# Optimization experiments

Hardware: AMD Instinct MI355X
Metric: run time of the kernel (lower is better)

Reference implementation:

```python
import jax, jax.numpy as jnp
import numpy as np

B = 4096          # batch_size (pairs); 2B total rows
D = 512           # embedding dim
TEMPERATURE = 0.5 # registered buffer in the torch module
EPS = 1e-12       # F.normalize eps


def _l2_normalize(x):
    # torch F.normalize: x / max(||x||_2, eps)
    n = jnp.sqrt(jnp.sum(x * x, axis=1, keepdims=True))
    return x / jnp.maximum(n, EPS)


def setup_inputs() -> dict:
    key = jax.random.key(0)
    k1, k2 = jax.random.split(key)
    return {
        "emb_i": jax.random.normal(k1, (B, D), dtype=jnp.float32),
        "emb_j": jax.random.normal(k2, (B, D), dtype=jnp.float32),
    }


def reference(emb_i, emb_j):
    z_i = _l2_normalize(emb_i)                     # [B, D]
    z_j = _l2_normalize(emb_j)                     # [B, D]
    z = jnp.concatenate([z_i, z_j], axis=0)        # [2B, D]
    # cosine similarity of normalized rows == plain GEMM (instead of the
    # broadcasted unsqueeze in the original, same math)
    sim = z @ z.T                                  # [2B, 2B]
    positives = jnp.concatenate(
        [jnp.diagonal(sim, offset=B), jnp.diagonal(sim, offset=-B)], axis=0
    )                                              # [2B]
    nominator = jnp.exp(positives / TEMPERATURE)   # [2B]
    # NOTE: the original multiplies exp(sim/T) by an *identity* mask (a bug
    # w.r.t. SimCLR, but we reproduce it faithfully): the row-sum of
    # eye * exp(sim/T) is exactly exp(diag(sim)/T).
    denominator = jnp.exp(jnp.diagonal(sim) / TEMPERATURE)  # [2B]
    loss_partial = -jnp.log(nominator / denominator)         # [2B]
    loss = jnp.sum(loss_partial) / (2 * B)
    return loss
```

## Files before the change

### kernel.cpp

```cpp
#include <hip/hip_runtime.h>
#include <hip/hip_bf16.h>


#define BATCH 4096
#define DIM 512
#define ROWS_PER_BLOCK 4
#define NBLOCKS (BATCH / ROWS_PER_BLOCK)

__global__ void pair_cosine_partial(const float* __restrict__ a,
                                    const float* __restrict__ b,
                                    float* __restrict__ partial) {
    const int wave = threadIdx.x >> 6;
    const int lane = threadIdx.x & 63;
    const int row  = blockIdx.x * ROWS_PER_BLOCK + wave;

    const float4* a4 = reinterpret_cast<const float4*>(a) + (size_t)row * (DIM / 4);
    const float4* b4 = reinterpret_cast<const float4*>(b) + (size_t)row * (DIM / 4);

    float4 av0 = a4[lane];
    float4 av1 = a4[lane + 64];
    float4 bv0 = b4[lane];
    float4 bv1 = b4[lane + 64];

    float dot = av0.x * bv0.x + av0.y * bv0.y + av0.z * bv0.z + av0.w * bv0.w
              + av1.x * bv1.x + av1.y * bv1.y + av1.z * bv1.z + av1.w * bv1.w;
    float na  = av0.x * av0.x + av0.y * av0.y + av0.z * av0.z + av0.w * av0.w
              + av1.x * av1.x + av1.y * av1.y + av1.z * av1.z + av1.w * av1.w;
    float nb  = bv0.x * bv0.x + bv0.y * bv0.y + bv0.z * bv0.z + bv0.w * bv0.w
              + bv1.x * bv1.x + bv1.y * bv1.y + bv1.z * bv1.z + bv1.w * bv1.w;

    #pragma unroll
    for (int off = 32; off > 0; off >>= 1) {
        dot += __shfl_xor(dot, off);
        na  += __shfl_xor(na, off);
        nb  += __shfl_xor(nb, off);
    }

    __shared__ float s[ROWS_PER_BLOCK];
    if (lane == 0) {
        float denom = fmaxf(sqrtf(na), 1e-12f) * fmaxf(sqrtf(nb), 1e-12f);
        s[wave] = dot / denom;
    }
    __syncthreads();
    if (threadIdx.x == 0) {
        partial[blockIdx.x] = s[0] + s[1] + s[2] + s[3];
    }
}

__global__ void finalize_loss(const float* __restrict__ partial,
                              float* __restrict__ out) {
    const int t = threadIdx.x;
    float v = partial[t] + partial[t + 256] + partial[t + 512] + partial[t + 768];
    #pragma unroll
    for (int off = 32; off > 0; off >>= 1) {
        v += __shfl_xor(v, off);
    }
    __shared__ float s[4];
    if ((t & 63) == 0) s[t >> 6] = v;
    __syncthreads();
    if (t == 0) {
        float sum_p = s[0] + s[1] + s[2] + s[3];
        float mean_p = sum_p / (float)BATCH;
        out[0] = (1.0f - mean_p) * 2.0f;
    }
}

extern "C" void kernel_launch(void* const* d_in, const int* in_sizes, int n_in,
                              void* d_out, int out_size, void* d_ws, size_t ws_size,
                              hipStream_t stream) {
    const float* a = (const float*)d_in[0];
    const float* b = (const float*)d_in[1];
    float* out = (float*)d_out;
    float* partial = (float*)d_ws;

    pair_cosine_partial<<<NBLOCKS, 256, 0, stream>>>(a, b, partial);
    finalize_loss<<<1, 256, 0, stream>>>(partial, out);
}
```

Baseline: 11.41 us.

## Fuse partial and finalize kernels via cooperative grid sync

Merges the per-pair cosine kernel and the final reduction kernel into one cooperative kernel that uses a grid-wide sync before block 0 reduces the partials. Blocks grow to 1024 threads, 16 rows each, so 256 blocks are launched. The aim is to remove the second launch and its gap. In exchange it pays for a grid barrier and the cost of a cooperative launch, and it needs all 256 blocks to be co-resident on the GPU.

```diff
diff --git a/kernel.cpp b/kernel.cpp
--- a/kernel.cpp
+++ b/kernel.cpp
@@ -1,18 +1,23 @@
 #include <hip/hip_runtime.h>
-#include <hip/hip_bf16.h>
+#include <hip/hip_cooperative_groups.h>
+
+namespace cg = cooperative_groups;
 
 
 #define BATCH 4096
 #define DIM 512
-#define ROWS_PER_BLOCK 4
-#define NBLOCKS (BATCH / ROWS_PER_BLOCK)
+#define THREADS 1024
+#define WAVES_PER_BLOCK 16
+#define NBLOCKS (BATCH / WAVES_PER_BLOCK)
 
-__global__ void pair_cosine_partial(const float* __restrict__ a,
-                                    const float* __restrict__ b,
-                                    float* __restrict__ partial) {
+__global__ void __launch_bounds__(THREADS)
+fused_contrastive_loss(const float* __restrict__ a,
+                       const float* __restrict__ b,
+                       float* __restrict__ out,
+                       float* __restrict__ partial) {
     const int wave = threadIdx.x >> 6;
     const int lane = threadIdx.x & 63;
-    const int row  = blockIdx.x * ROWS_PER_BLOCK + wave;
+    const int row  = blockIdx.x * WAVES_PER_BLOCK + wave;
 
     const float4* a4 = reinterpret_cast<const float4*>(a) + (size_t)row * (DIM / 4);
     const float4* b4 = reinterpret_cast<const float4*>(b) + (size_t)row * (DIM / 4);
@@ -36,32 +41,37 @@
         nb  += __shfl_xor(nb, off);
     }
 
-    __shared__ float s[ROWS_PER_BLOCK];
+    __shared__ float s[WAVES_PER_BLOCK];
     if (lane == 0) {
         float denom = fmaxf(sqrtf(na), 1e-12f) * fmaxf(sqrtf(nb), 1e-12f);
         s[wave] = dot / denom;
     }
     __syncthreads();
     if (threadIdx.x == 0) {
-        partial[blockIdx.x] = s[0] + s[1] + s[2] + s[3];
+        float p = 0.f;
+        #pragma unroll
+        for (int i = 0; i < WAVES_PER_BLOCK; ++i) p += s[i];
+        partial[blockIdx.x] = p;
     }
-}
 
-__global__ void finalize_loss(const float* __restrict__ partial,
-                              float* __restrict__ out) {
-    const int t = threadIdx.x;
-    float v = partial[t] + partial[t + 256] + partial[t + 512] + partial[t + 768];
-    #pragma unroll
-    for (int off = 32; off > 0; off >>= 1) {
-        v += __shfl_xor(v, off);
-    }
-    __shared__ float s[4];
-    if ((t & 63) == 0) s[t >> 6] = v;
-    __syncthreads();
-    if (t == 0) {
-        float sum_p = s[0] + s[1] + s[2] + s[3];
-        float mean_p = sum_p / (float)BATCH;
-        out[0] = (1.0f - mean_p) * 2.0f;
+    cg::this_grid().sync();
+
+    if (blockIdx.x == 0) {
+        float v = (threadIdx.x < NBLOCKS) ? partial[threadIdx.x] : 0.0f;
+        #pragma unroll
+        for (int off = 32; off > 0; off >>= 1) {
+            v += __shfl_xor(v, off);
+        }
+        __shared__ float s2[WAVES_PER_BLOCK];
+        if (lane == 0) s2[wave] = v;
+        __syncthreads();
+        if (threadIdx.x == 0) {
+            float sum_p = 0.f;
+            #pragma unroll
+            for (int i = 0; i < WAVES_PER_BLOCK; ++i) sum_p += s2[i];
+            float mean_p = sum_p / (float)BATCH;
+            out[0] = (1.0f - mean_p) * 2.0f;
+        }
     }
 }
 
@@ -73,6 +83,7 @@
     float* out = (float*)d_out;
     float* partial = (float*)d_ws;
 
-    pair_cosine_partial<<<NBLOCKS, 256, 0, stream>>>(a, b, partial);
-    finalize_loss<<<1, 256, 0, stream>>>(partial, out);
+    void* args[] = {(void*)&a, (void*)&b, (void*)&out, (void*)&partial};
+    hipLaunchCooperativeKernel((const void*)fused_contrastive_loss,
+                               dim3(NBLOCKS), dim3(THREADS), args, 0, stream);
 }
```

After: 39.01 us. 242% more time.
